# Optimization experiments

Measured on AMD Instinct MI355X. Metric: run time of the kernel, lower is better.

The kernel has to match this reference:

```python
import jax, jax.numpy as jnp
import numpy as np

B, M, K, F_IN, H = 64, 1024, 16, 4, 64  # B graphs of M nodes each, k=16 neighbors


def _knn_idx(h):
    # h: [B, M, H] -> indices of K nearest neighbors (excluding self): [B, M, K]
    sq = jnp.sum(h * h, axis=-1)                                   # [B, M]
    d = sq[:, :, None] + sq[:, None, :] - 2.0 * jnp.einsum('bmf,bnf->bmn', h, h)
    d = jnp.where(jnp.eye(M, dtype=bool)[None], jnp.float32(jnp.inf), d)
    _, idx = jax.lax.top_k(-d, K)                                  # smallest distances
    return idx


def _edge_conv(h, w1, b1, w2, b2):
    # Dynamic-graph EdgeConv with max aggregation (PyG default):
    # msg = MLP(concat[x_i, x_j - x_i]); out_i = max_j msg
    idx = _knn_idx(h)                                              # [B, M, K]
    x_j = jax.vmap(lambda hb, ib: hb[ib])(h, idx)                  # [B, M, K, H]
    x_i = jnp.broadcast_to(h[:, :, None, :], x_j.shape)
    msg = jnp.concatenate([x_i, x_j - x_i], axis=-1)               # [B, M, K, 2H]
    msg = jax.nn.relu(msg @ w1 + b1) @ w2 + b2                     # [B, M, K, H]
    return jnp.max(msg, axis=2)                                    # [B, M, H]


def setup_inputs() -> dict:
    key = jax.random.key(0)
    ks = jax.random.split(key, 20)

    def lin(k, fi, fo):
        return jax.random.normal(k, (fi, fo), jnp.float32) / np.sqrt(fi)

    inp = {
        'x': jax.random.normal(ks[0], (B * M, F_IN), jnp.float32),
        'batch': jnp.repeat(jnp.arange(B, dtype=jnp.int64), M),
        # encoder: Linear(4,32) ReLU Linear(32,64) ReLU
        'enc_w1': lin(ks[1], F_IN, 32), 'enc_b1': jnp.zeros((32,), jnp.float32),
        'enc_w2': lin(ks[2], 32, H),    'enc_b2': jnp.zeros((H,), jnp.float32),
        # EdgeConv MLPs: Linear(128,64) ReLU Linear(64,64)
        'ec1_w1': lin(ks[3], 2 * H, H), 'ec1_b1': jnp.zeros((H,), jnp.float32),
        'ec1_w2': lin(ks[4], H, H),     'ec1_b2': jnp.zeros((H,), jnp.float32),
        'ec2_w1': lin(ks[5], 2 * H, H), 'ec2_b1': jnp.zeros((H,), jnp.float32),
        'ec2_w2': lin(ks[6], H, H),     'ec2_b2': jnp.zeros((H,), jnp.float32),
        # output MLP: Linear(64,32) ReLU Linear(32,1)
        'out_w1': lin(ks[7], H, 32),    'out_b1': jnp.zeros((32,), jnp.float32),
        'out_w2': lin(ks[8], 32, 1),    'out_b2': jnp.zeros((1,), jnp.float32),
    }
    return inp


def reference(x, batch, enc_w1, enc_b1, enc_w2, enc_b2,
              ec1_w1, ec1_b1, ec1_w2, ec1_b2,
              ec2_w1, ec2_b1, ec2_w2, ec2_b2,
              out_w1, out_b1, out_w2, out_b2):
    # batch is repeat(arange(B), M): equal-size graphs -> reshape into [B, M, .]
    h = jax.nn.relu(jax.nn.relu(x @ enc_w1 + enc_b1) @ enc_w2 + enc_b2)  # [N, 64]
    h = h.reshape(B, M, H)
    h = _edge_conv(h, ec1_w1, ec1_b1, ec1_w2, ec1_b2)
    h = _edge_conv(h, ec2_w1, ec2_b1, ec2_w2, ec2_b2)
    g = jnp.mean(h, axis=1)                                        # global_mean_pool -> [B, 64]
    out = jax.nn.relu(g @ out_w1 + out_b1) @ out_w2 + out_b2       # [B, 1]
    return out.reshape(-1)                                         # [B]
```

## Files before the change

### kernel.cpp

```cpp
#include <hip/hip_runtime.h>
#include <math.h>

#define B_ 64
#define M_ 1024
#define H_ 64
#define N_ (B_*M_)

typedef _Float16 half8 __attribute__((ext_vector_type(8)));
typedef float  floatx4 __attribute__((ext_vector_type(4)));

#define MFMA16(a,b,c) __builtin_amdgcn_mfma_f32_16x16x32_f16(a,b,c,0,0,0)
#define MED3(a,b,c)   __builtin_amdgcn_fmed3f(a,b,c)

__global__ __launch_bounds__(256) void enc_kernel(
    const float* __restrict__ x,
    const float* __restrict__ w1,
    const float* __restrict__ b1,
    const float* __restrict__ w2,
    const float* __restrict__ b2,
    float* __restrict__ h,
    _Float16* __restrict__ hhi,
    _Float16* __restrict__ hlo,
    float* __restrict__ sq)
{
    __shared__ float sw1[4*32];
    __shared__ float sb1[32];
    __shared__ float sw2[32*64];
    __shared__ float sb2[64];
    int t = threadIdx.x;
    for (int i = t; i < 128; i += 256) sw1[i] = w1[i];
    if (t < 32) sb1[t] = b1[t];
    for (int i = t; i < 2048; i += 256) sw2[i] = w2[i];
    if (t < 64) sb2[t] = b2[t];
    __syncthreads();
    int n = blockIdx.x * 256 + t;
    float4 xv = *(const float4*)(x + (size_t)n*4);
    float hid[32];
    #pragma unroll
    for (int o = 0; o < 32; ++o) {
        float a = sb1[o] + xv.x*sw1[0*32+o] + xv.y*sw1[1*32+o]
                        + xv.z*sw1[2*32+o] + xv.w*sw1[3*32+o];
        hid[o] = fmaxf(a, 0.f);
    }
    float* hout = h + (size_t)n*64;
    float sqa = 0.f;
    #pragma unroll 4
    for (int oc = 0; oc < 16; ++oc) {
        float4 acc = make_float4(sb2[oc*4+0], sb2[oc*4+1], sb2[oc*4+2], sb2[oc*4+3]);
        #pragma unroll
        for (int f = 0; f < 32; ++f) {
            float4 w = *(const float4*)(sw2 + f*64 + oc*4);
            float hv = hid[f];
            acc.x += hv*w.x; acc.y += hv*w.y; acc.z += hv*w.z; acc.w += hv*w.w;
        }
        acc.x = fmaxf(acc.x,0.f); acc.y = fmaxf(acc.y,0.f);
        acc.z = fmaxf(acc.z,0.f); acc.w = fmaxf(acc.w,0.f);
        *(float4*)(hout + oc*4) = acc;
        sqa += acc.x*acc.x + acc.y*acc.y + acc.z*acc.z + acc.w*acc.w;
        union { _Float16 f[4]; uint2 u; } Hh, Hl;
        Hh.f[0]=(_Float16)acc.x; Hh.f[1]=(_Float16)acc.y;
        Hh.f[2]=(_Float16)acc.z; Hh.f[3]=(_Float16)acc.w;
        Hl.f[0]=(_Float16)(acc.x-(float)Hh.f[0]); Hl.f[1]=(_Float16)(acc.y-(float)Hh.f[1]);
        Hl.f[2]=(_Float16)(acc.z-(float)Hh.f[2]); Hl.f[3]=(_Float16)(acc.w-(float)Hh.f[3]);
        *(uint2*)(hhi + (size_t)n*64 + oc*4) = Hh.u;
        *(uint2*)(hlo + (size_t)n*64 + oc*4) = Hl.u;
    }
    sq[n] = sqa;
}

__global__ __launch_bounds__(256) void convert_kernel(
    const float* __restrict__ h,
    _Float16* __restrict__ hhi, _Float16* __restrict__ hlo,
    float* __restrict__ sq)
{
    int t = threadIdx.x, lane = t & 63, w = t >> 6;
    int base = blockIdx.x * 64 + w * 16;
    for (int it = 0; it < 16; ++it) {
        int i = base + it;
        float v = h[(size_t)i*64 + lane];
        _Float16 hi = (_Float16)v;
        _Float16 lo = (_Float16)(v - (float)hi);
        hhi[(size_t)i*64 + lane] = hi;
        hlo[(size_t)i*64 + lane] = lo;
        float s = v*v;
        #pragma unroll
        for (int off = 1; off < 64; off <<= 1) s += __shfl_xor(s, off, 64);
        if (lane == 0) sq[i] = s;
    }
}

__global__ __launch_bounds__(256) void gemmA_kernel(
    const float* __restrict__ h,
    const float* __restrict__ w1,
    float* __restrict__ A)
{
    __shared__ float sw[64*64];
    int t = threadIdx.x;
    for (int idx = t; idx < 4096; idx += 256) sw[idx] = w1[4096 + idx];
    __syncthreads();
    int n = blockIdx.x * 256 + t;
    float4 hv[16];
    const float* src = h + (size_t)n*64;
    #pragma unroll
    for (int c = 0; c < 16; ++c) hv[c] = *(const float4*)(src + c*4);
    float* dst = A + (size_t)n*64;
    #pragma unroll 2
    for (int oc = 0; oc < 16; ++oc) {
        float4 acc = make_float4(0.f,0.f,0.f,0.f);
        #pragma unroll
        for (int f = 0; f < 64; ++f) {
            float xv = ((const float*)hv)[f];
            float4 w = *(const float4*)(sw + f*64 + oc*4);
            acc.x += xv*w.x; acc.y += xv*w.y; acc.z += xv*w.z; acc.w += xv*w.w;
        }
        *(float4*)(dst + oc*4) = acc;
    }
}

__global__ __launch_bounds__(256, 4) void knn_kernel(
    const _Float16* __restrict__ hhi,
    const _Float16* __restrict__ hlo,
    const float* __restrict__ sqg,
    unsigned short* __restrict__ knn)
{
    __shared__ __align__(16) _Float16 bufH[2][16*64];
    __shared__ __align__(16) _Float16 bufL[2][16*64];
    __shared__ __align__(16) float sqS[1024];
    __shared__ float md[64*65];

    int t = threadIdx.x, lane = t & 63, w = t >> 6;
    int bi = blockIdx.x;
    int g  = (bi & 7) | ((bi >> 7) << 3);
    int qt = (bi >> 3) & 15;
    const _Float16* hhig = hhi + (size_t)g*M_*64;
    const _Float16* hlog = hlo + (size_t)g*M_*64;
    const float*    sqb  = sqg + (size_t)g*M_;

    ((float4*)sqS)[t] = ((const float4*)sqb)[t];

    int m16 = lane & 15, gid = lane >> 4;
    int crow = gid*4, koct = gid*8;
    int sw = m16 & 7;

    int rr = (w & 1)*8 + (lane >> 3);
    int gl = lane & 7;
    int pp = gl ^ (rr & 7);
    const _Float16* srcb = (w < 2 ? hhig : hlog) + rr*64 + gl*8;
    int dsto = rr*64 + pp*8;
    _Float16* db0 = (w < 2 ? bufH[0] : bufL[0]) + dsto;
    _Float16* db1 = (w < 2 ? bufH[1] : bufL[1]) + dsto;

    half8 Qh0, Qh1, Ql0, Ql1;
    {
        const _Float16* ph = hhig + (size_t)(qt*64 + w*16 + m16)*64;
        const _Float16* pl = hlog + (size_t)(qt*64 + w*16 + m16)*64;
        Qh0 = *(const half8*)(ph + koct);
        Qh1 = *(const half8*)(ph + 32 + koct);
        Ql0 = *(const half8*)(pl + koct);
        Ql1 = *(const half8*)(pl + 32 + koct);
    }

    float bd[16];
    #pragma unroll
    for (int k = 0; k < 16; ++k) bd[k] = INFINITY;

    int t_self = qt*4 + w;

    float4 ldA = *(const float4*)(srcb);
    float4 ldB = *(const float4*)(srcb + 1024);
    *(float4*)db0 = ldA;
    ldA = *(const float4*)(srcb + 2*1024);
    __syncthreads();

    float c1 = 1.f + sqS[qt*64 + w*16 + m16];

    int o0 = m16*64 + ((gid ^ sw) * 8);
    int o1 = o0 ^ 32;

    auto compute = [&](int T, const _Float16* bh, const _Float16* bl) {
        half8 Ah0 = *(const half8*)(bh + o0);
        half8 Ah1 = *(const half8*)(bh + o1);
        half8 Al0 = *(const half8*)(bl + o0);
        half8 Al1 = *(const half8*)(bl + o1);
        floatx4 acc = {0.f, 0.f, 0.f, 0.f};
        acc = MFMA16(Ah0, Qh0, acc);
        acc = MFMA16(Ah1, Qh1, acc);
        acc = MFMA16(Ah0, Ql0, acc);
        acc = MFMA16(Ah1, Ql1, acc);
        acc = MFMA16(Al0, Qh0, acc);
        acc = MFMA16(Al1, Qh1, acc);
        float4 sqv = *(const float4*)(sqS + T*16 + crow);
        unsigned cid = (unsigned)(T*16 + crow);
        bool st = (T == t_self);
        #pragma unroll
        for (int r = 0; r < 4; ++r) {
            float s  = fmaf(-2.f, acc[r], (&sqv.x)[r]);
            float t2 = c1 + s;
            unsigned kb = (__float_as_uint(t2) & 0xFFFFFC00u) | (cid + r);
            float fk = __uint_as_float(kb);
            if (st && (crow + r) == m16) fk = INFINITY;
            float nb0 = fminf(bd[0], fk);
            #pragma unroll
            for (int k = 15; k >= 1; --k) bd[k] = MED3(fk, bd[k-1], bd[k]);
            bd[0] = nb0;
        }
    };

    #pragma unroll 1
    for (int T = 0; T < 64; T += 2) {
        __builtin_amdgcn_s_barrier();
        *(float4*)db1 = ldB;
        ldB = *(const float4*)(srcb + (size_t)((T+3)&63)*1024);
        asm volatile("s_waitcnt lgkmcnt(0)" ::: "memory");
        __builtin_amdgcn_s_barrier();
        __builtin_amdgcn_sched_barrier(0);
        compute(T, bufH[0], bufL[0]);
        __builtin_amdgcn_s_barrier();
        *(float4*)db0 = ldA;
        ldA = *(const float4*)(srcb + (size_t)((T+4)&63)*1024);
        asm volatile("s_waitcnt lgkmcnt(0)" ::: "memory");
        __builtin_amdgcn_s_barrier();
        __builtin_amdgcn_sched_barrier(0);
        compute(T+1, bufH[1], bufL[1]);
    }

    int qrow = w*16 + m16;
    #pragma unroll
    for (int k = 0; k < 16; ++k) md[qrow*65 + gid*16 + k] = bd[k];
    __syncthreads();
    if (w == 0) {
        float b2[16];
        #pragma unroll
        for (int k = 0; k < 16; ++k) b2[k] = INFINITY;
        const float* mrow = md + lane*65;
        #pragma unroll
        for (int c8 = 0; c8 < 8; ++c8) {
            float sv[8];
            #pragma unroll
            for (int j = 0; j < 8; ++j) sv[j] = mrow[c8*8 + j];
            #pragma unroll
            for (int j = 0; j < 8; ++j) {
                float s = sv[j];
                float nb0 = fminf(b2[0], s);
                #pragma unroll
                for (int k = 15; k >= 1; --k) b2[k] = MED3(s, b2[k-1], b2[k]);
                b2[0] = nb0;
            }
        }
        union { unsigned short us[16]; uint4 v4[2]; } o;
        #pragma unroll
        for (int k = 0; k < 16; ++k)
            o.us[k] = (unsigned short)(__float_as_uint(b2[k]) & 1023u);
        size_t gq = (size_t)g*M_ + qt*64 + lane;
        uint4* dst = (uint4*)(knn + gq*16);
        dst[0] = o.v4[0];
        dst[1] = o.v4[1];
    }
}

__global__ __launch_bounds__(256) void edge_kernel(
    const float* __restrict__ h,
    const float* __restrict__ A,
    const unsigned short* __restrict__ knn,
    const float* __restrict__ w1,
    const float* __restrict__ b1,
    const float* __restrict__ w2,
    const float* __restrict__ b2,
    float* __restrict__ hout)
{
    __shared__ __align__(16) _Float16 wdf[16*64*8];
    __shared__ __align__(16) _Float16 w2f[16*64*8];
    float* CsB = (float*)w2f;
    int t = threadIdx.x;
    for (int u = t; u < 512; u += 256) {
        int ulane = u & 63, nt = u >> 7, ks = (u >> 6) & 1;
        int n = nt*16 + (ulane & 15);
        int kbase = ks*32 + ((ulane >> 4) * 8);
        int fh = (((nt*2+ks)*2+0)*64 + ulane)*8;
        int fl = (((nt*2+ks)*2+1)*64 + ulane)*8;
        #pragma unroll
        for (int j = 0; j < 8; ++j) {
            int k = kbase + j;
            float vd = w1[k*64+n] - w1[4096 + k*64+n];
            _Float16 dh = (_Float16)vd;
            wdf[fh+j] = dh;
            wdf[fl+j] = (_Float16)(vd - (float)dh);
            float v2 = w2[k*64+n];
            _Float16 h2 = (_Float16)v2;
            w2f[fh+j] = h2;
            w2f[fl+j] = (_Float16)(v2 - (float)h2);
        }
    }
    __syncthreads();
    int lane = t & 63, wid = t >> 6;
    int m16 = lane & 15, gid = lane >> 4;
    int koct = gid*8, crow = gid*4;
    int bi = blockIdx.x;
    int g  = (bi & 7) | ((bi >> 7) << 3);
    int qt = (bi >> 3) & 15;
    int i0 = g*M_ + qt*64 + wid*16;
    const float* Ab = A + (size_t)g*M_*H_;

    half8 W2r[4][2][2];
    #pragma unroll
    for (int nt = 0; nt < 4; ++nt)
        #pragma unroll
        for (int ks = 0; ks < 2; ++ks)
            #pragma unroll
            for (int p = 0; p < 2; ++p)
                W2r[nt][ks][p] = *(const half8*)&w2f[(((nt*2+ks)*2+p)*64+lane)*8];

    float b1v[4];
    #pragma unroll
    for (int nt = 0; nt < 4; ++nt) b1v[nt] = b1[nt*16+m16];
    float b2v = b2[gid*16+m16];
    __syncthreads();

    half8 Hh[2], Hl[2];
    #pragma unroll
    for (int ks = 0; ks < 2; ++ks) {
        const float* hp = h + (size_t)(i0+m16)*64 + ks*32 + koct;
        float4 v0 = *(const float4*)hp;
        float4 v1 = *(const float4*)(hp+4);
        float va[8] = {v0.x,v0.y,v0.z,v0.w,v1.x,v1.y,v1.z,v1.w};
        #pragma unroll
        for (int j = 0; j < 8; ++j) {
            _Float16 hi = (_Float16)va[j];
            Hh[ks][j] = hi;
            Hl[ks][j] = (_Float16)(va[j]-(float)hi);
        }
    }
    #pragma unroll
    for (int nt = 0; nt < 4; ++nt) {
        floatx4 acc = {b1v[nt], b1v[nt], b1v[nt], b1v[nt]};
        #pragma unroll
        for (int ks = 0; ks < 2; ++ks) {
            half8 wh = *(const half8*)&wdf[(((nt*2+ks)*2+0)*64+lane)*8];
            half8 wl = *(const half8*)&wdf[(((nt*2+ks)*2+1)*64+lane)*8];
            acc = MFMA16(Hh[ks], wh, acc);
            acc = MFMA16(Hh[ks], wl, acc);
            acc = MFMA16(Hl[ks], wh, acc);
        }
        #pragma unroll
        for (int r = 0; r < 4; ++r)
            CsB[((wid*16) + crow + r)*64 + nt*16 + m16] = acc[r];
    }
    __syncthreads();

    const unsigned short* knb = knn + (size_t)i0*16;
    #pragma unroll 2
    for (int nn = 0; nn < 16; ++nn) {
        int j = knb[nn*16 + m16];
        const float* Ap = Ab + (size_t)j*64;
        half8 Mh[2], Ml[2];
        #pragma unroll
        for (int ks = 0; ks < 2; ++ks) {
            float4 a0 = *(const float4*)(Ap + ks*32 + koct);
            float4 a1 = *(const float4*)(Ap + ks*32 + koct + 4);
            const float* cp = &CsB[(wid*16 + nn)*64 + ks*32 + koct];
            float4 c0 = *(const float4*)cp;
            float4 c1 = *(const float4*)(cp+4);
            float mv[8] = {
                fmaxf(a0.x+c0.x,0.f), fmaxf(a0.y+c0.y,0.f),
                fmaxf(a0.z+c0.z,0.f), fmaxf(a0.w+c0.w,0.f),
                fmaxf(a1.x+c1.x,0.f), fmaxf(a1.y+c1.y,0.f),
                fmaxf(a1.z+c1.z,0.f), fmaxf(a1.w+c1.w,0.f)};
            #pragma unroll
            for (int jj = 0; jj < 8; ++jj) {
                _Float16 hi = (_Float16)mv[jj];
                Mh[ks][jj] = hi;
                Ml[ks][jj] = (_Float16)(mv[jj]-(float)hi);
            }
        }
        floatx4 acc[4];
        #pragma unroll
        for (int nt = 0; nt < 4; ++nt) {
            acc[nt] = (floatx4){0.f,0.f,0.f,0.f};
            #pragma unroll
            for (int ks = 0; ks < 2; ++ks) {
                acc[nt] = MFMA16(Mh[ks], W2r[nt][ks][0], acc[nt]);
                acc[nt] = MFMA16(Mh[ks], W2r[nt][ks][1], acc[nt]);
                acc[nt] = MFMA16(Ml[ks], W2r[nt][ks][0], acc[nt]);
            }
        }
        float om[4];
        #pragma unroll
        for (int nt = 0; nt < 4; ++nt) {
            float mr = fmaxf(fmaxf(acc[nt][0], acc[nt][1]),
                             fmaxf(acc[nt][2], acc[nt][3]));
            mr = fmaxf(mr, __shfl_xor(mr, 16, 64));
            mr = fmaxf(mr, __shfl_xor(mr, 32, 64));
            om[nt] = mr;
        }
        float val = (gid == 0) ? om[0] : (gid == 1) ? om[1]
                  : (gid == 2) ? om[2] : om[3];
        hout[(size_t)(i0+nn)*64 + gid*16 + m16] = val + b2v;
    }
}

__global__ __launch_bounds__(256) void pool_kernel(
    const float* __restrict__ h,
    const float* __restrict__ w1,
    const float* __restrict__ b1,
    const float* __restrict__ w2,
    const float* __restrict__ b2,
    float* __restrict__ out)
{
    __shared__ float part[4][64];
    __shared__ float g[64];
    __shared__ float hid[32];
    int t = threadIdx.x;
    int o = t & 63, p = t >> 6;
    int b = blockIdx.x;
    const float* hb = h + (size_t)b*M_*H_;
    float s = 0.f;
    for (int m = p; m < M_; m += 4) s += hb[(size_t)m*64 + o];
    part[p][o] = s;
    __syncthreads();
    if (t < 64) g[t] = (part[0][t] + part[1][t] + part[2][t] + part[3][t]) * (1.f/M_);
    __syncthreads();
    if (t < 32) {
        float a = b1[t];
        for (int f = 0; f < 64; ++f) a += g[f] * w1[f*32 + t];
        hid[t] = fmaxf(a, 0.f);
    }
    __syncthreads();
    if (t == 0) {
        float a = b2[0];
        for (int f = 0; f < 32; ++f) a += hid[f] * w2[f];
        out[b] = a;
    }
}

extern "C" void kernel_launch(void* const* d_in, const int* in_sizes, int n_in,
                              void* d_out, int out_size, void* d_ws, size_t ws_size,
                              hipStream_t stream)
{
    (void)in_sizes; (void)n_in; (void)out_size; (void)ws_size;
    const float* x      = (const float*)d_in[0];
    const float* enc_w1 = (const float*)d_in[2];
    const float* enc_b1 = (const float*)d_in[3];
    const float* enc_w2 = (const float*)d_in[4];
    const float* enc_b2 = (const float*)d_in[5];
    const float* ec1_w1 = (const float*)d_in[6];
    const float* ec1_b1 = (const float*)d_in[7];
    const float* ec1_w2 = (const float*)d_in[8];
    const float* ec1_b2 = (const float*)d_in[9];
    const float* ec2_w1 = (const float*)d_in[10];
    const float* ec2_b1 = (const float*)d_in[11];
    const float* ec2_w2 = (const float*)d_in[12];
    const float* ec2_b2 = (const float*)d_in[13];
    const float* out_w1 = (const float*)d_in[14];
    const float* out_b1 = (const float*)d_in[15];
    const float* out_w2 = (const float*)d_in[16];
    const float* out_b2 = (const float*)d_in[17];

    char* ws = (char*)d_ws;
    float*          h   = (float*)(ws);
    char*           r2  = ws + (size_t)N_*64*4;
    _Float16*       hhi = (_Float16*)r2;
    _Float16*       hlo = (_Float16*)(r2 + (size_t)N_*64*2);
    float*          A   = (float*)r2;
    unsigned short* idx = (unsigned short*)(ws + (size_t)N_*64*4*2);
    float*          sq  = (float*)(ws + (size_t)N_*64*4*2 + (size_t)N_*16*2);

    enc_kernel<<<N_/256, 256, 0, stream>>>(x, enc_w1, enc_b1, enc_w2, enc_b2,
                                           h, hhi, hlo, sq);
    knn_kernel <<<B_*16, 256, 0, stream>>>(hhi, hlo, sq, idx);
    gemmA_kernel<<<N_/256, 256, 0, stream>>>(h, ec1_w1, A);
    edge_kernel<<<N_/64, 256, 0, stream>>>(h, A, idx, ec1_w1, ec1_b1, ec1_w2, ec1_b2, h);
    convert_kernel<<<N_/64, 256, 0, stream>>>(h, hhi, hlo, sq);
    knn_kernel <<<B_*16, 256, 0, stream>>>(hhi, hlo, sq, idx);
    gemmA_kernel<<<N_/256, 256, 0, stream>>>(h, ec2_w1, A);
    edge_kernel<<<N_/64, 256, 0, stream>>>(h, A, idx, ec2_w1, ec2_b1, ec2_w2, ec2_b2, h);
    pool_kernel<<<B_, 256, 0, stream>>>(h, out_w1, out_b1, out_w2, out_b2, (float*)d_out);
}
```

Measured before the change: 413.5 us.

## Load kNN candidate tiles directly from global into registers, drop LDS staging

Removes the shared-memory double buffer and its per-tile barriers from the kNN kernel. Each wave now loads its candidate fragments (hi/lo halves) straight from global memory into registers, prefetching the next tile while computing the current one. This eliminates LDS writes, reads and block-wide synchronisation. In exchange, every wave loads the same candidate tile separately (4x redundant global/L2 traffic) and uses more registers.

```diff
diff --git a/kernel.cpp b/kernel.cpp
--- a/kernel.cpp
+++ b/kernel.cpp
@@ -123,8 +123,6 @@
     const float* __restrict__ sqg,
     unsigned short* __restrict__ knn)
 {
-    __shared__ __align__(16) _Float16 bufH[2][16*64];
-    __shared__ __align__(16) _Float16 bufL[2][16*64];
     __shared__ __align__(16) float sqS[1024];
     __shared__ float md[64*65];
 
@@ -140,15 +138,7 @@
 
     int m16 = lane & 15, gid = lane >> 4;
     int crow = gid*4, koct = gid*8;
-    int sw = m16 & 7;
-
-    int rr = (w & 1)*8 + (lane >> 3);
-    int gl = lane & 7;
-    int pp = gl ^ (rr & 7);
-    const _Float16* srcb = (w < 2 ? hhig : hlog) + rr*64 + gl*8;
-    int dsto = rr*64 + pp*8;
-    _Float16* db0 = (w < 2 ? bufH[0] : bufL[0]) + dsto;
-    _Float16* db1 = (w < 2 ? bufH[1] : bufL[1]) + dsto;
+    int rowoff = m16*64 + koct;
 
     half8 Qh0, Qh1, Ql0, Ql1;
     {
@@ -166,29 +156,32 @@
 
     int t_self = qt*4 + w;
 
-    float4 ldA = *(const float4*)(srcb);
-    float4 ldB = *(const float4*)(srcb + 1024);
-    *(float4*)db0 = ldA;
-    ldA = *(const float4*)(srcb + 2*1024);
-    __syncthreads();
-
+    half8 cH0, cH1, cL0, cL1, nH0, nH1, nL0, nL1;
+    {
+        const _Float16* ph = hhig + rowoff;
+        const _Float16* pl = hlog + rowoff;
+        cH0 = *(const half8*)ph;  cH1 = *(const half8*)(ph + 32);
+        cL0 = *(const half8*)pl;  cL1 = *(const half8*)(pl + 32);
+    }
+    __syncthreads();
     float c1 = 1.f + sqS[qt*64 + w*16 + m16];
 
-    int o0 = m16*64 + ((gid ^ sw) * 8);
-    int o1 = o0 ^ 32;
-
-    auto compute = [&](int T, const _Float16* bh, const _Float16* bl) {
-        half8 Ah0 = *(const half8*)(bh + o0);
-        half8 Ah1 = *(const half8*)(bh + o1);
-        half8 Al0 = *(const half8*)(bl + o0);
-        half8 Al1 = *(const half8*)(bl + o1);
+    #pragma unroll 2
+    for (int T = 0; T < 64; ++T) {
+        {
+            size_t o = (size_t)((T+1) & 63) * 1024 + rowoff;
+            const _Float16* ph = hhig + o;
+            const _Float16* pl = hlog + o;
+            nH0 = *(const half8*)ph;  nH1 = *(const half8*)(ph + 32);
+            nL0 = *(const half8*)pl;  nL1 = *(const half8*)(pl + 32);
+        }
         floatx4 acc = {0.f, 0.f, 0.f, 0.f};
-        acc = MFMA16(Ah0, Qh0, acc);
-        acc = MFMA16(Ah1, Qh1, acc);
-        acc = MFMA16(Ah0, Ql0, acc);
-        acc = MFMA16(Ah1, Ql1, acc);
-        acc = MFMA16(Al0, Qh0, acc);
-        acc = MFMA16(Al1, Qh1, acc);
+        acc = MFMA16(cH0, Qh0, acc);
+        acc = MFMA16(cH1, Qh1, acc);
+        acc = MFMA16(cH0, Ql0, acc);
+        acc = MFMA16(cH1, Ql1, acc);
+        acc = MFMA16(cL0, Qh0, acc);
+        acc = MFMA16(cL1, Qh1, acc);
         float4 sqv = *(const float4*)(sqS + T*16 + crow);
         unsigned cid = (unsigned)(T*16 + crow);
         bool st = (T == t_self);
@@ -204,24 +197,7 @@
             for (int k = 15; k >= 1; --k) bd[k] = MED3(fk, bd[k-1], bd[k]);
             bd[0] = nb0;
         }
-    };
-
-    #pragma unroll 1
-    for (int T = 0; T < 64; T += 2) {
-        __builtin_amdgcn_s_barrier();
-        *(float4*)db1 = ldB;
-        ldB = *(const float4*)(srcb + (size_t)((T+3)&63)*1024);
-        asm volatile("s_waitcnt lgkmcnt(0)" ::: "memory");
-        __builtin_amdgcn_s_barrier();
-        __builtin_amdgcn_sched_barrier(0);
-        compute(T, bufH[0], bufL[0]);
-        __builtin_amdgcn_s_barrier();
-        *(float4*)db0 = ldA;
-        ldA = *(const float4*)(srcb + (size_t)((T+4)&63)*1024);
-        asm volatile("s_waitcnt lgkmcnt(0)" ::: "memory");
-        __builtin_amdgcn_s_barrier();
-        __builtin_amdgcn_sched_barrier(0);
-        compute(T+1, bufH[1], bufL[1]);
+        cH0 = nH0; cH1 = nH1; cL0 = nL0; cL1 = nL1;
     }
 
     int qrow = w*16 + m16;
```

Result: slower. 531.3 us (+28.5%).

## Double query rows per kNN block to reuse candidate tiles across two query groups

Applied to the files above, without the earlier changes.

Each kNN block now handles 128 query rows instead of 64: every wave holds two 16-row query fragments and two independent top-16 lists, and each staged candidate tile (now 32 rows) feeds both. This halves the grid and halves redundant global/LDS loading of candidate tiles per query, and lets MFMA work for one query group overlap with the sorting-network inserts of the other. In exchange it doubles per-thread register state (occupancy hint lowered to 2 blocks/CU) and LDS use, and the grid drops to 512 blocks, which may underfill the GPU.

```diff
diff --git a/kernel.cpp b/kernel.cpp
--- a/kernel.cpp
+++ b/kernel.cpp
@@ -117,21 +117,21 @@
     }
 }
 
-__global__ __launch_bounds__(256, 4) void knn_kernel(
+__global__ __launch_bounds__(256, 2) void knn_kernel(
     const _Float16* __restrict__ hhi,
     const _Float16* __restrict__ hlo,
     const float* __restrict__ sqg,
     unsigned short* __restrict__ knn)
 {
-    __shared__ __align__(16) _Float16 bufH[2][16*64];
-    __shared__ __align__(16) _Float16 bufL[2][16*64];
+    __shared__ __align__(16) _Float16 bufH[2][32*64];
+    __shared__ __align__(16) _Float16 bufL[2][32*64];
     __shared__ __align__(16) float sqS[1024];
-    __shared__ float md[64*65];
+    __shared__ float md[128*65];
 
     int t = threadIdx.x, lane = t & 63, w = t >> 6;
     int bi = blockIdx.x;
-    int g  = (bi & 7) | ((bi >> 7) << 3);
-    int qt = (bi >> 3) & 15;
+    int g   = (bi & 7) | ((bi >> 6) << 3);
+    int qt8 = (bi >> 3) & 7;
     const _Float16* hhig = hhi + (size_t)g*M_*64;
     const _Float16* hlog = hlo + (size_t)g*M_*64;
     const float*    sqb  = sqg + (size_t)g*M_;
@@ -142,97 +142,135 @@
     int crow = gid*4, koct = gid*8;
     int sw = m16 & 7;
 
-    int rr = (w & 1)*8 + (lane >> 3);
-    int gl = lane & 7;
+    int u  = ((w & 1) << 6) | lane;
+    int rr = u >> 3;
+    int gl = u & 7;
     int pp = gl ^ (rr & 7);
     const _Float16* srcb = (w < 2 ? hhig : hlog) + rr*64 + gl*8;
-    int dsto = rr*64 + pp*8;
-    _Float16* db0 = (w < 2 ? bufH[0] : bufL[0]) + dsto;
-    _Float16* db1 = (w < 2 ? bufH[1] : bufL[1]) + dsto;
-
-    half8 Qh0, Qh1, Ql0, Ql1;
+    _Float16* dst0 = (w < 2 ? bufH[0] : bufL[0]) + rr*64 + pp*8;
+    _Float16* dst1 = (w < 2 ? bufH[1] : bufL[1]) + rr*64 + pp*8;
+
+    int qbase = qt8*128 + w*32;
+    half8 Q0h0, Q0h1, Q0l0, Q0l1, Q1h0, Q1h1, Q1l0, Q1l1;
     {
-        const _Float16* ph = hhig + (size_t)(qt*64 + w*16 + m16)*64;
-        const _Float16* pl = hlog + (size_t)(qt*64 + w*16 + m16)*64;
-        Qh0 = *(const half8*)(ph + koct);
-        Qh1 = *(const half8*)(ph + 32 + koct);
-        Ql0 = *(const half8*)(pl + koct);
-        Ql1 = *(const half8*)(pl + 32 + koct);
-    }
-
-    float bd[16];
-    #pragma unroll
-    for (int k = 0; k < 16; ++k) bd[k] = INFINITY;
-
-    int t_self = qt*4 + w;
-
-    float4 ldA = *(const float4*)(srcb);
-    float4 ldB = *(const float4*)(srcb + 1024);
-    *(float4*)db0 = ldA;
-    ldA = *(const float4*)(srcb + 2*1024);
-    __syncthreads();
-
-    float c1 = 1.f + sqS[qt*64 + w*16 + m16];
+        const _Float16* ph = hhig + (size_t)(qbase + m16)*64;
+        const _Float16* pl = hlog + (size_t)(qbase + m16)*64;
+        Q0h0 = *(const half8*)(ph + koct);
+        Q0h1 = *(const half8*)(ph + 32 + koct);
+        Q0l0 = *(const half8*)(pl + koct);
+        Q0l1 = *(const half8*)(pl + 32 + koct);
+        ph += 16*64; pl += 16*64;
+        Q1h0 = *(const half8*)(ph + koct);
+        Q1h1 = *(const half8*)(ph + 32 + koct);
+        Q1l0 = *(const half8*)(pl + koct);
+        Q1l1 = *(const half8*)(pl + 32 + koct);
+    }
+
+    float bd0[16], bd1[16];
+    #pragma unroll
+    for (int k = 0; k < 16; ++k) { bd0[k] = INFINITY; bd1[k] = INFINITY; }
+
+    int ts0 = qt8*8 + w*2;
+    int ts1 = ts0 + 1;
+
+    float4 a0, a1, b0, b1;
+    a0 = *(const float4*)(srcb);
+    a1 = *(const float4*)(srcb + 1024);
+    b0 = *(const float4*)(srcb + 2048);
+    b1 = *(const float4*)(srcb + 3072);
+    *(float4*)dst0 = a0;  *(float4*)(dst0 + 1024) = a1;
+    a0 = *(const float4*)(srcb + 2*2048);
+    a1 = *(const float4*)(srcb + 2*2048 + 1024);
+    __syncthreads();
+
+    float c10 = 1.f + sqS[qbase + m16];
+    float c11 = 1.f + sqS[qbase + 16 + m16];
 
     int o0 = m16*64 + ((gid ^ sw) * 8);
     int o1 = o0 ^ 32;
 
-    auto compute = [&](int T, const _Float16* bh, const _Float16* bl) {
-        half8 Ah0 = *(const half8*)(bh + o0);
-        half8 Ah1 = *(const half8*)(bh + o1);
-        half8 Al0 = *(const half8*)(bl + o0);
-        half8 Al1 = *(const half8*)(bl + o1);
-        floatx4 acc = {0.f, 0.f, 0.f, 0.f};
-        acc = MFMA16(Ah0, Qh0, acc);
-        acc = MFMA16(Ah1, Qh1, acc);
-        acc = MFMA16(Ah0, Ql0, acc);
-        acc = MFMA16(Ah1, Ql1, acc);
-        acc = MFMA16(Al0, Qh0, acc);
-        acc = MFMA16(Al1, Qh1, acc);
-        float4 sqv = *(const float4*)(sqS + T*16 + crow);
-        unsigned cid = (unsigned)(T*16 + crow);
-        bool st = (T == t_self);
+    auto insert4 = [&](float (&bdr)[16], floatx4 acc, float4 sqv,
+                       unsigned cid, bool st, float c1v) {
         #pragma unroll
         for (int r = 0; r < 4; ++r) {
             float s  = fmaf(-2.f, acc[r], (&sqv.x)[r]);
-            float t2 = c1 + s;
+            float t2 = c1v + s;
             unsigned kb = (__float_as_uint(t2) & 0xFFFFFC00u) | (cid + r);
             float fk = __uint_as_float(kb);
             if (st && (crow + r) == m16) fk = INFINITY;
-            float nb0 = fminf(bd[0], fk);
+            float nb0 = fminf(bdr[0], fk);
             #pragma unroll
-            for (int k = 15; k >= 1; --k) bd[k] = MED3(fk, bd[k-1], bd[k]);
-            bd[0] = nb0;
+            for (int k = 15; k >= 1; --k) bdr[k] = MED3(fk, bdr[k-1], bdr[k]);
+            bdr[0] = nb0;
         }
     };
 
+    auto compute = [&](int T, const _Float16* bh, const _Float16* bl) {
+        #pragma unroll
+        for (int s = 0; s < 2; ++s) {
+            int ob = s*1024;
+            half8 Ah0 = *(const half8*)(bh + ob + o0);
+            half8 Ah1 = *(const half8*)(bh + ob + o1);
+            half8 Al0 = *(const half8*)(bl + ob + o0);
+            half8 Al1 = *(const half8*)(bl + ob + o1);
+            float4 sqv = *(const float4*)(sqS + T*32 + s*16 + crow);
+            unsigned cid = (unsigned)(T*32 + s*16 + crow);
+            int ts = T*2 + s;
+            floatx4 acc = {0.f, 0.f, 0.f, 0.f};
+            acc = MFMA16(Ah0, Q0h0, acc);
+            acc = MFMA16(Ah1, Q0h1, acc);
+            acc = MFMA16(Ah0, Q0l0, acc);
+            acc = MFMA16(Ah1, Q0l1, acc);
+            acc = MFMA16(Al0, Q0h0, acc);
+            acc = MFMA16(Al1, Q0h1, acc);
+            insert4(bd0, acc, sqv, cid, ts == ts0, c10);
+            floatx4 acc2 = {0.f, 0.f, 0.f, 0.f};
+            acc2 = MFMA16(Ah0, Q1h0, acc2);
+            acc2 = MFMA16(Ah1, Q1h1, acc2);
+            acc2 = MFMA16(Ah0, Q1l0, acc2);
+            acc2 = MFMA16(Ah1, Q1l1, acc2);
+            acc2 = MFMA16(Al0, Q1h0, acc2);
+            acc2 = MFMA16(Al1, Q1h1, acc2);
+            insert4(bd1, acc2, sqv, cid, ts == ts1, c11);
+        }
+    };
+
     #pragma unroll 1
-    for (int T = 0; T < 64; T += 2) {
+    for (int T = 0; T < 32; T += 2) {
         __builtin_amdgcn_s_barrier();
-        *(float4*)db1 = ldB;
-        ldB = *(const float4*)(srcb + (size_t)((T+3)&63)*1024);
+        *(float4*)dst1 = b0;  *(float4*)(dst1 + 1024) = b1;
+        { size_t o = (size_t)((T+3)&31)*2048;
+          b0 = *(const float4*)(srcb + o);
+          b1 = *(const float4*)(srcb + o + 1024); }
         asm volatile("s_waitcnt lgkmcnt(0)" ::: "memory");
         __builtin_amdgcn_s_barrier();
         __builtin_amdgcn_sched_barrier(0);
         compute(T, bufH[0], bufL[0]);
         __builtin_amdgcn_s_barrier();
-        *(float4*)db0 = ldA;
-        ldA = *(const float4*)(srcb + (size_t)((T+4)&63)*1024);
+        *(float4*)dst0 = a0;  *(float4*)(dst0 + 1024) = a1;
+        { size_t o = (size_t)((T+4)&31)*2048;
+          a0 = *(const float4*)(srcb + o);
+          a1 = *(const float4*)(srcb + o + 1024); }
         asm volatile("s_waitcnt lgkmcnt(0)" ::: "memory");
         __builtin_amdgcn_s_barrier();
         __builtin_amdgcn_sched_barrier(0);
         compute(T+1, bufH[1], bufL[1]);
     }
 
-    int qrow = w*16 + m16;
-    #pragma unroll
-    for (int k = 0; k < 16; ++k) md[qrow*65 + gid*16 + k] = bd[k];
-    __syncthreads();
-    if (w == 0) {
+    __syncthreads();
+    int qrow0 = w*32 + m16;
+    #pragma unroll
+    for (int k = 0; k < 16; ++k) {
+        md[qrow0*65 + gid*16 + k]      = bd0[k];
+        md[(qrow0+16)*65 + gid*16 + k] = bd1[k];
+    }
+    __syncthreads();
+    if (w < 2) {
+        int q = w*64 + lane;
         float b2[16];
         #pragma unroll
         for (int k = 0; k < 16; ++k) b2[k] = INFINITY;
-        const float* mrow = md + lane*65;
+        const float* mrow = md + (size_t)q*65;
         #pragma unroll
         for (int c8 = 0; c8 < 8; ++c8) {
             float sv[8];
@@ -251,7 +289,7 @@
         #pragma unroll
         for (int k = 0; k < 16; ++k)
             o.us[k] = (unsigned short)(__float_as_uint(b2[k]) & 1023u);
-        size_t gq = (size_t)g*M_ + qt*64 + lane;
+        size_t gq = (size_t)g*M_ + qt8*128 + q;
         uint4* dst = (uint4*)(knn + gq*16);
         dst[0] = o.v4[0];
         dst[1] = o.v4[1];
@@ -466,11 +504,11 @@
 
     enc_kernel<<<N_/256, 256, 0, stream>>>(x, enc_w1, enc_b1, enc_w2, enc_b2,
                                            h, hhi, hlo, sq);
-    knn_kernel <<<B_*16, 256, 0, stream>>>(hhi, hlo, sq, idx);
+    knn_kernel <<<B_*8, 256, 0, stream>>>(hhi, hlo, sq, idx);
     gemmA_kernel<<<N_/256, 256, 0, stream>>>(h, ec1_w1, A);
     edge_kernel<<<N_/64, 256, 0, stream>>>(h, A, idx, ec1_w1, ec1_b1, ec1_w2, ec1_b2, h);
     convert_kernel<<<N_/64, 256, 0, stream>>>(h, hhi, hlo, sq);
-    knn_kernel <<<B_*16, 256, 0, stream>>>(hhi, hlo, sq, idx);
+    knn_kernel <<<B_*8, 256, 0, stream>>>(hhi, hlo, sq, idx);
     gemmA_kernel<<<N_/256, 256, 0, stream>>>(h, ec2_w1, A);
     edge_kernel<<<N_/64, 256, 0, stream>>>(h, A, idx, ec2_w1, ec2_b1, ec2_w2, ec2_b2, h);
     pool_kernel<<<B_, 256, 0, stream>>>(h, out_w1, out_b1, out_w2, out_b2, (float*)d_out);
```

Result: faster. 403.7 us (-2.4%).

## Enlarge knn tiles to 128 queries and 32 candidates per block with 512 threads

Applied to the files above, without the earlier changes.

The knn kernel now uses 512-thread blocks that each handle 128 query rows and stage 32 candidate rows per pipeline step instead of 16. This halves the block count and the number of barrier-separated steps, so each candidate row loaded into shared memory serves twice as many queries. In exchange it uses more shared memory and runs a heavier final merge per block, which can lower occupancy and leave fewer blocks to spread across the GPU.

```diff
diff --git a/kernel.cpp b/kernel.cpp
--- a/kernel.cpp
+++ b/kernel.cpp
@@ -117,43 +117,44 @@
     }
 }
 
-__global__ __launch_bounds__(256, 4) void knn_kernel(
+__global__ __launch_bounds__(512, 4) void knn_kernel(
     const _Float16* __restrict__ hhi,
     const _Float16* __restrict__ hlo,
     const float* __restrict__ sqg,
     unsigned short* __restrict__ knn)
 {
-    __shared__ __align__(16) _Float16 bufH[2][16*64];
-    __shared__ __align__(16) _Float16 bufL[2][16*64];
+    __shared__ __align__(16) _Float16 bufH[2][32*64];
+    __shared__ __align__(16) _Float16 bufL[2][32*64];
     __shared__ __align__(16) float sqS[1024];
-    __shared__ float md[64*65];
+    __shared__ float md[128*65];
 
     int t = threadIdx.x, lane = t & 63, w = t >> 6;
     int bi = blockIdx.x;
-    int g  = (bi & 7) | ((bi >> 7) << 3);
-    int qt = (bi >> 3) & 15;
+    int g   = (bi & 7) | ((bi >> 6) << 3);
+    int qt8 = (bi >> 3) & 7;
     const _Float16* hhig = hhi + (size_t)g*M_*64;
     const _Float16* hlog = hlo + (size_t)g*M_*64;
     const float*    sqb  = sqg + (size_t)g*M_;
 
-    ((float4*)sqS)[t] = ((const float4*)sqb)[t];
+    if (t < 256) ((float4*)sqS)[t] = ((const float4*)sqb)[t];
 
     int m16 = lane & 15, gid = lane >> 4;
     int crow = gid*4, koct = gid*8;
     int sw = m16 & 7;
 
-    int rr = (w & 1)*8 + (lane >> 3);
-    int gl = lane & 7;
+    int u  = t & 255;
+    int rr = u >> 3;
+    int gl = u & 7;
     int pp = gl ^ (rr & 7);
-    const _Float16* srcb = (w < 2 ? hhig : hlog) + rr*64 + gl*8;
-    int dsto = rr*64 + pp*8;
-    _Float16* db0 = (w < 2 ? bufH[0] : bufL[0]) + dsto;
-    _Float16* db1 = (w < 2 ? bufH[1] : bufL[1]) + dsto;
-
+    const _Float16* srcb = (t < 256 ? hhig : hlog) + rr*64 + gl*8;
+    _Float16* dst0 = (t < 256 ? bufH[0] : bufL[0]) + rr*64 + pp*8;
+    _Float16* dst1 = (t < 256 ? bufH[1] : bufL[1]) + rr*64 + pp*8;
+
+    int qbase = qt8*128 + w*16;
     half8 Qh0, Qh1, Ql0, Ql1;
     {
-        const _Float16* ph = hhig + (size_t)(qt*64 + w*16 + m16)*64;
-        const _Float16* pl = hlog + (size_t)(qt*64 + w*16 + m16)*64;
+        const _Float16* ph = hhig + (size_t)(qbase + m16)*64;
+        const _Float16* pl = hlog + (size_t)(qbase + m16)*64;
         Qh0 = *(const half8*)(ph + koct);
         Qh1 = *(const half8*)(ph + 32 + koct);
         Ql0 = *(const half8*)(pl + koct);
@@ -164,34 +165,21 @@
     #pragma unroll
     for (int k = 0; k < 16; ++k) bd[k] = INFINITY;
 
-    int t_self = qt*4 + w;
-
-    float4 ldA = *(const float4*)(srcb);
-    float4 ldB = *(const float4*)(srcb + 1024);
-    *(float4*)db0 = ldA;
-    ldA = *(const float4*)(srcb + 2*1024);
-    __syncthreads();
-
-    float c1 = 1.f + sqS[qt*64 + w*16 + m16];
+    int ts_self = qt8*8 + w;
+
+    float4 a, b;
+    a = *(const float4*)(srcb);
+    b = *(const float4*)(srcb + 2048);
+    *(float4*)dst0 = a;
+    a = *(const float4*)(srcb + 2*2048);
+    __syncthreads();
+
+    float c1 = 1.f + sqS[qbase + m16];
 
     int o0 = m16*64 + ((gid ^ sw) * 8);
     int o1 = o0 ^ 32;
 
-    auto compute = [&](int T, const _Float16* bh, const _Float16* bl) {
-        half8 Ah0 = *(const half8*)(bh + o0);
-        half8 Ah1 = *(const half8*)(bh + o1);
-        half8 Al0 = *(const half8*)(bl + o0);
-        half8 Al1 = *(const half8*)(bl + o1);
-        floatx4 acc = {0.f, 0.f, 0.f, 0.f};
-        acc = MFMA16(Ah0, Qh0, acc);
-        acc = MFMA16(Ah1, Qh1, acc);
-        acc = MFMA16(Ah0, Ql0, acc);
-        acc = MFMA16(Ah1, Ql1, acc);
-        acc = MFMA16(Al0, Qh0, acc);
-        acc = MFMA16(Al1, Qh1, acc);
-        float4 sqv = *(const float4*)(sqS + T*16 + crow);
-        unsigned cid = (unsigned)(T*16 + crow);
-        bool st = (T == t_self);
+    auto insert4 = [&](floatx4 acc, float4 sqv, unsigned cid, bool st) {
         #pragma unroll
         for (int r = 0; r < 4; ++r) {
             float s  = fmaf(-2.f, acc[r], (&sqv.x)[r]);
@@ -206,33 +194,57 @@
         }
     };
 
+    auto compute = [&](int T, const _Float16* bh, const _Float16* bl) {
+        #pragma unroll
+        for (int s = 0; s < 2; ++s) {
+            int ob = s*1024;
+            half8 Ah0 = *(const half8*)(bh + ob + o0);
+            half8 Ah1 = *(const half8*)(bh + ob + o1);
+            half8 Al0 = *(const half8*)(bl + ob + o0);
+            half8 Al1 = *(const half8*)(bl + ob + o1);
+            float4 sqv = *(const float4*)(sqS + T*32 + s*16 + crow);
+            unsigned cid = (unsigned)(T*32 + s*16 + crow);
+            bool st = (T*2 + s) == ts_self;
+            floatx4 acc = {0.f, 0.f, 0.f, 0.f};
+            acc = MFMA16(Ah0, Qh0, acc);
+            acc = MFMA16(Ah1, Qh1, acc);
+            acc = MFMA16(Ah0, Ql0, acc);
+            acc = MFMA16(Ah1, Ql1, acc);
+            acc = MFMA16(Al0, Qh0, acc);
+            acc = MFMA16(Al1, Qh1, acc);
+            insert4(acc, sqv, cid, st);
+        }
+    };
+
     #pragma unroll 1
-    for (int T = 0; T < 64; T += 2) {
+    for (int T = 0; T < 32; T += 2) {
         __builtin_amdgcn_s_barrier();
-        *(float4*)db1 = ldB;
-        ldB = *(const float4*)(srcb + (size_t)((T+3)&63)*1024);
+        *(float4*)dst1 = b;
+        b = *(const float4*)(srcb + (size_t)((T+3)&31)*2048);
         asm volatile("s_waitcnt lgkmcnt(0)" ::: "memory");
         __builtin_amdgcn_s_barrier();
         __builtin_amdgcn_sched_barrier(0);
         compute(T, bufH[0], bufL[0]);
         __builtin_amdgcn_s_barrier();
-        *(float4*)db0 = ldA;
-        ldA = *(const float4*)(srcb + (size_t)((T+4)&63)*1024);
+        *(float4*)dst0 = a;
+        a = *(const float4*)(srcb + (size_t)((T+4)&31)*2048);
         asm volatile("s_waitcnt lgkmcnt(0)" ::: "memory");
         __builtin_amdgcn_s_barrier();
         __builtin_amdgcn_sched_barrier(0);
         compute(T+1, bufH[1], bufL[1]);
     }
 
+    __syncthreads();
     int qrow = w*16 + m16;
     #pragma unroll
     for (int k = 0; k < 16; ++k) md[qrow*65 + gid*16 + k] = bd[k];
     __syncthreads();
-    if (w == 0) {
+    if (w < 2) {
+        int q = w*64 + lane;
         float b2[16];
         #pragma unroll
         for (int k = 0; k < 16; ++k) b2[k] = INFINITY;
-        const float* mrow = md + lane*65;
+        const float* mrow = md + (size_t)q*65;
         #pragma unroll
         for (int c8 = 0; c8 < 8; ++c8) {
             float sv[8];
@@ -251,7 +263,7 @@
         #pragma unroll
         for (int k = 0; k < 16; ++k)
             o.us[k] = (unsigned short)(__float_as_uint(b2[k]) & 1023u);
-        size_t gq = (size_t)g*M_ + qt*64 + lane;
+        size_t gq = (size_t)g*M_ + qt8*128 + q;
         uint4* dst = (uint4*)(knn + gq*16);
         dst[0] = o.v4[0];
         dst[1] = o.v4[1];
@@ -466,11 +478,11 @@
 
     enc_kernel<<<N_/256, 256, 0, stream>>>(x, enc_w1, enc_b1, enc_w2, enc_b2,
                                            h, hhi, hlo, sq);
-    knn_kernel <<<B_*16, 256, 0, stream>>>(hhi, hlo, sq, idx);
+    knn_kernel <<<B_*8, 512, 0, stream>>>(hhi, hlo, sq, idx);
     gemmA_kernel<<<N_/256, 256, 0, stream>>>(h, ec1_w1, A);
     edge_kernel<<<N_/64, 256, 0, stream>>>(h, A, idx, ec1_w1, ec1_b1, ec1_w2, ec1_b2, h);
     convert_kernel<<<N_/64, 256, 0, stream>>>(h, hhi, hlo, sq);
-    knn_kernel <<<B_*16, 256, 0, stream>>>(hhi, hlo, sq, idx);
+    knn_kernel <<<B_*8, 512, 0, stream>>>(hhi, hlo, sq, idx);
     gemmA_kernel<<<N_/256, 256, 0, stream>>>(h, ec2_w1, A);
     edge_kernel<<<N_/64, 256, 0, stream>>>(h, A, idx, ec2_w1, ec2_b1, ec2_w2, ec2_b2, h);
     pool_kernel<<<B_, 256, 0, stream>>>(h, out_w1, out_b1, out_w2, out_b2, (float*)d_out);
```

Measured after the change: 404.1 us. 2.3% less time.
